# Kernel tuning notes

Measured on AMD Instinct MI355X. Metric: run time of the kernel, lower is better.

Reference implementation:

```python
import jax, jax.numpy as jnp
import numpy as np

N = 8192
F_IN = 512
F_OUT = 512
DENSITY = 0.01


def setup_inputs() -> dict:
    key = jax.random.key(0)
    k_x, k_adj, k_w, k_b = jax.random.split(key, 4)
    input_features = jax.random.normal(k_x, (N, F_IN), dtype=jnp.float32)
    adj = (jax.random.uniform(k_adj, (N, N)) < DENSITY).astype(jnp.float32)
    idx = jnp.arange(N)
    adj = adj.at[idx, idx].set(1.0)
    # nn.Linear(in, out) params; W stored as [in, out] so hidden = x @ W + b
    W = jax.random.normal(k_w, (F_IN, F_OUT), dtype=jnp.float32) / np.sqrt(F_IN)
    b = jax.random.normal(k_b, (F_OUT,), dtype=jnp.float32) * 0.01
    return {"input_features": input_features, "adj": adj, "W": W, "b": b}


def reference(input_features, adj, W, b):
    # adj.to_dense().bool().float(): binarize any nonzero entry
    A = (adj != 0).astype(input_features.dtype)  # [N, N]
    hidden = input_features @ W + b              # [N, F_out]
    deg = jnp.sum(A, axis=0)                     # column sums, [N]
    return (A @ hidden) / deg[:, None]           # [N, F_out]
```

## Files before the change

### kernel.cpp

```cpp
#include <hip/hip_runtime.h>
#include <stdint.h>

#define N_NODES 8192
#define FEAT 512
#define RCAP 192

__device__ __forceinline__ unsigned short f2bf(float f) {
  unsigned int u = __float_as_uint(f);
  u += 0x7fffu + ((u >> 16) & 1u);
  return (unsigned short)(u >> 16);
}
__device__ __forceinline__ float bflo(unsigned int u) { return __uint_as_float(u << 16); }
__device__ __forceinline__ float bfhi(unsigned int u) { return __uint_as_float(u & 0xffff0000u); }

typedef __attribute__((ext_vector_type(8))) short short8;
typedef __attribute__((ext_vector_type(4))) float floatx4;

__global__ __launch_bounds__(256) void prep_kernel(const float* __restrict__ W,
                                                   unsigned short* __restrict__ Wt,
                                                   unsigned int* __restrict__ deg) {
  int gid = blockIdx.x * 256 + threadIdx.x;
  int k = gid >> 9, n = gid & 511;
  Wt[n * 512 + k] = f2bf(W[gid]);
  if (gid < N_NODES) deg[gid] = 0u;
}

__global__ __launch_bounds__(512) void gemm_kernel(const float* __restrict__ x,
                                                   const unsigned short* __restrict__ Wt,
                                                   const float* __restrict__ bias,
                                                   unsigned short* __restrict__ hidden) {
  __shared__ __align__(16) unsigned short Ab[64][40];
  __shared__ __align__(16) unsigned short Bb[256][40];
  int t = threadIdx.x;
  int m0 = blockIdx.x * 64;
  int n0 = blockIdx.y * 256;
  int lane = t & 63, wave = t >> 6;
  int quad = lane >> 4, l15 = lane & 15;
  int wm = wave & 1, wn = wave >> 1;

  floatx4 acc[2][4];
#pragma unroll
  for (int i = 0; i < 2; ++i)
#pragma unroll
    for (int j = 0; j < 4; ++j) acc[i][j] = (floatx4)0.0f;

  int arow = t >> 3, ac = (t & 7) * 4;
  int brow = t >> 1, bc = (t & 1) * 16;
  const float* xa = x + (size_t)(m0 + arow) * 512 + ac;
  const unsigned short* wb = Wt + (size_t)(n0 + brow) * 512 + bc;

  for (int kt = 0; kt < 16; ++kt) {
    int k0 = kt * 32;
    __syncthreads();
    float4 av = *(const float4*)(xa + k0);
    uint2 aw;
    aw.x = (unsigned int)f2bf(av.x) | ((unsigned int)f2bf(av.y) << 16);
    aw.y = (unsigned int)f2bf(av.z) | ((unsigned int)f2bf(av.w) << 16);
    *(uint2*)&Ab[arow][ac] = aw;
    uint4 bv0 = *(const uint4*)(wb + k0);
    uint4 bv1 = *(const uint4*)(wb + k0 + 8);
    *(uint4*)&Bb[brow][bc] = bv0;
    *(uint4*)&Bb[brow][bc + 8] = bv1;
    __syncthreads();

    short8 af[2];
    short8 bfr[4];
#pragma unroll
    for (int im = 0; im < 2; ++im)
      af[im] = *(const short8*)&Ab[wm * 32 + im * 16 + l15][quad * 8];
#pragma unroll
    for (int jn = 0; jn < 4; ++jn)
      bfr[jn] = *(const short8*)&Bb[wn * 64 + jn * 16 + l15][quad * 8];
#pragma unroll
    for (int im = 0; im < 2; ++im)
#pragma unroll
      for (int jn = 0; jn < 4; ++jn)
        acc[im][jn] = __builtin_amdgcn_mfma_f32_16x16x32_bf16(af[im], bfr[jn], acc[im][jn], 0, 0, 0);
  }

#pragma unroll
  for (int jn = 0; jn < 4; ++jn) {
    int col = n0 + wn * 64 + jn * 16 + l15;
    float bb = bias[col];
#pragma unroll
    for (int im = 0; im < 2; ++im) {
#pragma unroll
      for (int rg = 0; rg < 4; ++rg) {
        int row = m0 + wm * 32 + im * 16 + quad * 4 + rg;
        hidden[(size_t)row * 512 + col] = f2bf(acc[im][jn][rg] + bb);
      }
    }
  }
}

#define SCAN4(cv, CH)                                                         \
  {                                                                           \
    int cbase = (CH) * 256 + 4 * lane;                                        \
    _Pragma("unroll")                                                         \
    for (int e = 0; e < 4; ++e) {                                             \
      float val = (e == 0) ? cv.x : (e == 1) ? cv.y : (e == 2) ? cv.z : cv.w; \
      bool nz = (val != 0.0f);                                                \
      unsigned long long m = __ballot(nz);                                    \
      if (nz) {                                                               \
        atomicAdd(&deg[cbase + e], 1u);                                       \
        int p = qcnt + __popcll(m & lanemask);                                \
        if (p < RCAP) row_idx[p] = (unsigned short)(cbase + e);               \
      }                                                                       \
      qcnt += __popcll(m);                                                    \
    }                                                                         \
  }

__global__ __launch_bounds__(256) void scan_kernel(const float* __restrict__ adj,
                                                   unsigned short* __restrict__ idx,
                                                   int* __restrict__ cnt,
                                                   unsigned int* __restrict__ deg) {
  int tid = threadIdx.x;
  int lane = tid & 63, wave = tid >> 6;
  unsigned long long lanemask = (1ull << lane) - 1ull;
  int r = blockIdx.x * 4 + wave;

  const float4* __restrict__ arow = (const float4*)(adj + ((size_t)r << 13));
  unsigned short* row_idx = idx + (size_t)r * RCAP;
  int qcnt = 0;

  float4 b0 = arow[0 * 64 + lane];
  float4 b1 = arow[1 * 64 + lane];
  float4 b2 = arow[2 * 64 + lane];
  float4 b3 = arow[3 * 64 + lane];
  for (int base = 0; base < 32; base += 4) {
    float4 c0 = b0, c1 = b1, c2 = b2, c3 = b3;
    if (base + 4 < 32) {
      b0 = arow[(base + 4) * 64 + lane];
      b1 = arow[(base + 5) * 64 + lane];
      b2 = arow[(base + 6) * 64 + lane];
      b3 = arow[(base + 7) * 64 + lane];
    }
    SCAN4(c0, base + 0)
    SCAN4(c1, base + 1)
    SCAN4(c2, base + 2)
    SCAN4(c3, base + 3)
  }
  if (lane == 0) cnt[r] = (qcnt < RCAP) ? qcnt : RCAP;
}

__global__ __launch_bounds__(256) void gather_kernel(const unsigned short* __restrict__ idx,
                                                     const int* __restrict__ cnt,
                                                     const unsigned int* __restrict__ deg,
                                                     const unsigned short* __restrict__ hidden,
                                                     float* __restrict__ out) {
  int tid = threadIdx.x;
  int lane = tid & 63, wave = tid >> 6;
  int r = blockIdx.x * 4 + wave;

  const unsigned short* ri = idx + (size_t)r * RCAP;
  int n = cnt[r];
  float acc[8] = {0.f, 0.f, 0.f, 0.f, 0.f, 0.f, 0.f, 0.f};

  uint4 iq = *(const uint4*)ri;
  int i = 0;
  for (; i + 8 <= n; i += 8) {
    uint4 iqn;
    if (i + 16 <= n) iqn = *(const uint4*)(ri + i + 8);
    int j[8];
    j[0] = iq.x & 0xffff; j[1] = iq.x >> 16;
    j[2] = iq.y & 0xffff; j[3] = iq.y >> 16;
    j[4] = iq.z & 0xffff; j[5] = iq.z >> 16;
    j[6] = iq.w & 0xffff; j[7] = iq.w >> 16;
    uint4 h[8];
#pragma unroll
    for (int d = 0; d < 8; ++d)
      h[d] = ((const uint4*)(hidden + ((size_t)j[d] << 9)))[lane];
#pragma unroll
    for (int d = 0; d < 8; ++d) {
      acc[0] += bflo(h[d].x); acc[1] += bfhi(h[d].x);
      acc[2] += bflo(h[d].y); acc[3] += bfhi(h[d].y);
      acc[4] += bflo(h[d].z); acc[5] += bfhi(h[d].z);
      acc[6] += bflo(h[d].w); acc[7] += bfhi(h[d].w);
    }
    iq = iqn;
  }
  for (; i < n; ++i) {
    int j = ri[i];
    uint4 h = ((const uint4*)(hidden + ((size_t)j << 9)))[lane];
    acc[0] += bflo(h.x); acc[1] += bfhi(h.x);
    acc[2] += bflo(h.y); acc[3] += bfhi(h.y);
    acc[4] += bflo(h.z); acc[5] += bfhi(h.z);
    acc[6] += bflo(h.w); acc[7] += bfhi(h.w);
  }

  float inv = 1.0f / (float)deg[r];
  float* orow = out + ((size_t)r << 9) + 8 * lane;
  *(float4*)orow       = make_float4(acc[0] * inv, acc[1] * inv, acc[2] * inv, acc[3] * inv);
  *(float4*)(orow + 4) = make_float4(acc[4] * inv, acc[5] * inv, acc[6] * inv, acc[7] * inv);
}

extern "C" void kernel_launch(void* const* d_in, const int* in_sizes, int n_in,
                              void* d_out, int out_size, void* d_ws, size_t ws_size,
                              hipStream_t stream) {
  const float* x   = (const float*)d_in[0];
  const float* adj = (const float*)d_in[1];
  const float* W   = (const float*)d_in[2];
  const float* b   = (const float*)d_in[3];
  float* out = (float*)d_out;

  char* ws = (char*)d_ws;
  unsigned short* hidden = (unsigned short*)ws;
  char* p = ws + (size_t)N_NODES * FEAT * 2;
  unsigned short* Wt = (unsigned short*)p;  p += (size_t)FEAT * FEAT * 2;
  unsigned int*   deg = (unsigned int*)p;   p += (size_t)N_NODES * 4;
  int*            cnt = (int*)p;            p += (size_t)N_NODES * 4;
  unsigned short* idx = (unsigned short*)p;

  prep_kernel<<<1024, 256, 0, stream>>>(W, Wt, deg);
  gemm_kernel<<<dim3(128, 2), 512, 0, stream>>>(x, Wt, b, hidden);
  scan_kernel<<<2048, 256, 0, stream>>>(adj, idx, cnt, deg);
  gather_kernel<<<2048, 256, 0, stream>>>(idx, cnt, deg, hidden, out);
}
```

Before: 448.2 us.

## Merge GEMM and adjacency scan into one launch, split gather by feature half

```diff
diff --git a/kernel.cpp b/kernel.cpp
--- a/kernel.cpp
+++ b/kernel.cpp
@@ -15,6 +15,9 @@
 
 typedef __attribute__((ext_vector_type(8))) short short8;
 typedef __attribute__((ext_vector_type(4))) float floatx4;
+typedef __attribute__((ext_vector_type(4))) float fvec4;
+typedef __attribute__((ext_vector_type(4))) unsigned int uvec4;
+typedef __attribute__((ext_vector_type(2))) unsigned int uvec2;
 
 __global__ __launch_bounds__(256) void prep_kernel(const float* __restrict__ W,
                                                    unsigned short* __restrict__ Wt,
@@ -25,16 +28,70 @@
   if (gid < N_NODES) deg[gid] = 0u;
 }
 
-__global__ __launch_bounds__(512) void gemm_kernel(const float* __restrict__ x,
-                                                   const unsigned short* __restrict__ Wt,
-                                                   const float* __restrict__ bias,
-                                                   unsigned short* __restrict__ hidden) {
+#define SCAN4(cv, CH)                                                         \
+  {                                                                           \
+    int cbase = (CH) * 256 + 4 * lane;                                        \
+    _Pragma("unroll")                                                         \
+    for (int e = 0; e < 4; ++e) {                                             \
+      float val = cv[e];                                                      \
+      bool nz = (val != 0.0f);                                                \
+      unsigned long long m = __ballot(nz);                                    \
+      if (nz) {                                                               \
+        atomicAdd(&deg[cbase + e], 1u);                                       \
+        int p = qcnt + __popcll(m & lanemask);                                \
+        if (p < RCAP)                                                         \
+          __builtin_nontemporal_store((unsigned short)(cbase + e),            \
+                                      row_idx + p);                           \
+      }                                                                       \
+      qcnt += __popcll(m);                                                    \
+    }                                                                         \
+  }
+
+__global__ __launch_bounds__(512, 4) void mega_kernel(const float* __restrict__ x,
+                                                      const unsigned short* __restrict__ Wt,
+                                                      const float* __restrict__ bias,
+                                                      unsigned short* __restrict__ hidden,
+                                                      const float* __restrict__ adj,
+                                                      unsigned short* __restrict__ idx,
+                                                      int* __restrict__ cnt,
+                                                      unsigned int* __restrict__ deg) {
   __shared__ __align__(16) unsigned short Ab[64][40];
   __shared__ __align__(16) unsigned short Bb[256][40];
+  int bid = blockIdx.x;
   int t = threadIdx.x;
-  int m0 = blockIdx.x * 64;
-  int n0 = blockIdx.y * 256;
   int lane = t & 63, wave = t >> 6;
+
+  if (bid < 1024) {
+    unsigned long long lanemask = (1ull << lane) - 1ull;
+    int r = bid * 8 + wave;
+    const fvec4* __restrict__ arow = (const fvec4*)(adj + ((size_t)r << 13));
+    unsigned short* row_idx = idx + (size_t)r * RCAP;
+    int qcnt = 0;
+
+    fvec4 b0 = __builtin_nontemporal_load(arow + 0 * 64 + lane);
+    fvec4 b1 = __builtin_nontemporal_load(arow + 1 * 64 + lane);
+    fvec4 b2 = __builtin_nontemporal_load(arow + 2 * 64 + lane);
+    fvec4 b3 = __builtin_nontemporal_load(arow + 3 * 64 + lane);
+    for (int base = 0; base < 32; base += 4) {
+      fvec4 c0 = b0, c1 = b1, c2 = b2, c3 = b3;
+      if (base + 4 < 32) {
+        b0 = __builtin_nontemporal_load(arow + (base + 4) * 64 + lane);
+        b1 = __builtin_nontemporal_load(arow + (base + 5) * 64 + lane);
+        b2 = __builtin_nontemporal_load(arow + (base + 6) * 64 + lane);
+        b3 = __builtin_nontemporal_load(arow + (base + 7) * 64 + lane);
+      }
+      SCAN4(c0, base + 0)
+      SCAN4(c1, base + 1)
+      SCAN4(c2, base + 2)
+      SCAN4(c3, base + 3)
+    }
+    if (lane == 0) cnt[r] = (qcnt < RCAP) ? qcnt : RCAP;
+    return;
+  }
+
+  int gb = bid - 1024;
+  int m0 = (gb >> 1) * 64;
+  int n0 = (gb & 1) * 256;
   int quad = lane >> 4, l15 = lane & 15;
   int wm = wave & 1, wn = wave >> 1;
 
@@ -44,10 +101,10 @@
 #pragma unroll
     for (int j = 0; j < 4; ++j) acc[i][j] = (floatx4)0.0f;
 
-  int arow = t >> 3, ac = (t & 7) * 4;
-  int brow = t >> 1, bc = (t & 1) * 16;
-  const float* xa = x + (size_t)(m0 + arow) * 512 + ac;
-  const unsigned short* wb = Wt + (size_t)(n0 + brow) * 512 + bc;
+  int arow_s = t >> 3, ac = (t & 7) * 4;
+  int brow_s = t >> 1, bc = (t & 1) * 16;
+  const float* xa = x + (size_t)(m0 + arow_s) * 512 + ac;
+  const unsigned short* wb = Wt + (size_t)(n0 + brow_s) * 512 + bc;
 
   for (int kt = 0; kt < 16; ++kt) {
     int k0 = kt * 32;
@@ -56,11 +113,11 @@
     uint2 aw;
     aw.x = (unsigned int)f2bf(av.x) | ((unsigned int)f2bf(av.y) << 16);
     aw.y = (unsigned int)f2bf(av.z) | ((unsigned int)f2bf(av.w) << 16);
-    *(uint2*)&Ab[arow][ac] = aw;
+    *(uint2*)&Ab[arow_s][ac] = aw;
     uint4 bv0 = *(const uint4*)(wb + k0);
     uint4 bv1 = *(const uint4*)(wb + k0 + 8);
-    *(uint4*)&Bb[brow][bc] = bv0;
-    *(uint4*)&Bb[brow][bc + 8] = bv1;
+    *(uint4*)&Bb[brow_s][bc] = bv0;
+    *(uint4*)&Bb[brow_s][bc + 8] = bv1;
     __syncthreads();
 
     short8 af[2];
@@ -93,105 +150,52 @@
   }
 }
 
-#define SCAN4(cv, CH)                                                         \
-  {                                                                           \
-    int cbase = (CH) * 256 + 4 * lane;                                        \
-    _Pragma("unroll")                                                         \
-    for (int e = 0; e < 4; ++e) {                                             \
-      float val = (e == 0) ? cv.x : (e == 1) ? cv.y : (e == 2) ? cv.z : cv.w; \
-      bool nz = (val != 0.0f);                                                \
-      unsigned long long m = __ballot(nz);                                    \
-      if (nz) {                                                               \
-        atomicAdd(&deg[cbase + e], 1u);                                       \
-        int p = qcnt + __popcll(m & lanemask);                                \
-        if (p < RCAP) row_idx[p] = (unsigned short)(cbase + e);               \
-      }                                                                       \
-      qcnt += __popcll(m);                                                    \
-    }                                                                         \
-  }
-
-__global__ __launch_bounds__(256) void scan_kernel(const float* __restrict__ adj,
-                                                   unsigned short* __restrict__ idx,
-                                                   int* __restrict__ cnt,
-                                                   unsigned int* __restrict__ deg) {
-  int tid = threadIdx.x;
-  int lane = tid & 63, wave = tid >> 6;
-  unsigned long long lanemask = (1ull << lane) - 1ull;
-  int r = blockIdx.x * 4 + wave;
-
-  const float4* __restrict__ arow = (const float4*)(adj + ((size_t)r << 13));
-  unsigned short* row_idx = idx + (size_t)r * RCAP;
-  int qcnt = 0;
-
-  float4 b0 = arow[0 * 64 + lane];
-  float4 b1 = arow[1 * 64 + lane];
-  float4 b2 = arow[2 * 64 + lane];
-  float4 b3 = arow[3 * 64 + lane];
-  for (int base = 0; base < 32; base += 4) {
-    float4 c0 = b0, c1 = b1, c2 = b2, c3 = b3;
-    if (base + 4 < 32) {
-      b0 = arow[(base + 4) * 64 + lane];
-      b1 = arow[(base + 5) * 64 + lane];
-      b2 = arow[(base + 6) * 64 + lane];
-      b3 = arow[(base + 7) * 64 + lane];
-    }
-    SCAN4(c0, base + 0)
-    SCAN4(c1, base + 1)
-    SCAN4(c2, base + 2)
-    SCAN4(c3, base + 3)
-  }
-  if (lane == 0) cnt[r] = (qcnt < RCAP) ? qcnt : RCAP;
-}
-
-__global__ __launch_bounds__(256) void gather_kernel(const unsigned short* __restrict__ idx,
-                                                     const int* __restrict__ cnt,
-                                                     const unsigned int* __restrict__ deg,
-                                                     const unsigned short* __restrict__ hidden,
-                                                     float* __restrict__ out) {
+__global__ __launch_bounds__(256, 7) void gather_kernel(const unsigned short* __restrict__ idx,
+                                                        const int* __restrict__ cnt,
+                                                        const unsigned int* __restrict__ deg,
+                                                        const unsigned short* __restrict__ hidden,
+                                                        float* __restrict__ out,
+                                                        int half) {
   int tid = threadIdx.x;
   int lane = tid & 63, wave = tid >> 6;
   int r = blockIdx.x * 4 + wave;
 
   const unsigned short* ri = idx + (size_t)r * RCAP;
   int n = cnt[r];
-  float acc[8] = {0.f, 0.f, 0.f, 0.f, 0.f, 0.f, 0.f, 0.f};
-
-  uint4 iq = *(const uint4*)ri;
+  float a0 = 0.f, a1 = 0.f, a2 = 0.f, a3 = 0.f;
+  const unsigned short* hbase = hidden + (half << 8) + 4 * lane;
+
+  uvec4 iq = __builtin_nontemporal_load((const uvec4*)ri);
   int i = 0;
   for (; i + 8 <= n; i += 8) {
-    uint4 iqn;
-    if (i + 16 <= n) iqn = *(const uint4*)(ri + i + 8);
+    uvec4 iqn = iq;
+    if (i + 16 <= n) iqn = __builtin_nontemporal_load((const uvec4*)(ri + i + 8));
     int j[8];
     j[0] = iq.x & 0xffff; j[1] = iq.x >> 16;
     j[2] = iq.y & 0xffff; j[3] = iq.y >> 16;
     j[4] = iq.z & 0xffff; j[5] = iq.z >> 16;
     j[6] = iq.w & 0xffff; j[7] = iq.w >> 16;
-    uint4 h[8];
+    uvec2 h[8];
 #pragma unroll
     for (int d = 0; d < 8; ++d)
-      h[d] = ((const uint4*)(hidden + ((size_t)j[d] << 9)))[lane];
+      h[d] = *(const uvec2*)(hbase + ((size_t)j[d] << 9));
 #pragma unroll
     for (int d = 0; d < 8; ++d) {
-      acc[0] += bflo(h[d].x); acc[1] += bfhi(h[d].x);
-      acc[2] += bflo(h[d].y); acc[3] += bfhi(h[d].y);
-      acc[4] += bflo(h[d].z); acc[5] += bfhi(h[d].z);
-      acc[6] += bflo(h[d].w); acc[7] += bfhi(h[d].w);
+      a0 += bflo(h[d].x); a1 += bfhi(h[d].x);
+      a2 += bflo(h[d].y); a3 += bfhi(h[d].y);
     }
     iq = iqn;
   }
   for (; i < n; ++i) {
     int j = ri[i];
-    uint4 h = ((const uint4*)(hidden + ((size_t)j << 9)))[lane];
-    acc[0] += bflo(h.x); acc[1] += bfhi(h.x);
-    acc[2] += bflo(h.y); acc[3] += bfhi(h.y);
-    acc[4] += bflo(h.z); acc[5] += bfhi(h.z);
-    acc[6] += bflo(h.w); acc[7] += bfhi(h.w);
+    uvec2 h = *(const uvec2*)(hbase + ((size_t)j << 9));
+    a0 += bflo(h.x); a1 += bfhi(h.x);
+    a2 += bflo(h.y); a3 += bfhi(h.y);
   }
 
   float inv = 1.0f / (float)deg[r];
-  float* orow = out + ((size_t)r << 9) + 8 * lane;
-  *(float4*)orow       = make_float4(acc[0] * inv, acc[1] * inv, acc[2] * inv, acc[3] * inv);
-  *(float4*)(orow + 4) = make_float4(acc[4] * inv, acc[5] * inv, acc[6] * inv, acc[7] * inv);
+  fvec4 o; o.x = a0 * inv; o.y = a1 * inv; o.z = a2 * inv; o.w = a3 * inv;
+  __builtin_nontemporal_store(o, (fvec4*)(out + ((size_t)r << 9) + (half << 8) + 4 * lane));
 }
 
 extern "C" void kernel_launch(void* const* d_in, const int* in_sizes, int n_in,
@@ -212,7 +216,7 @@
   unsigned short* idx = (unsigned short*)p;
 
   prep_kernel<<<1024, 256, 0, stream>>>(W, Wt, deg);
-  gemm_kernel<<<dim3(128, 2), 512, 0, stream>>>(x, Wt, b, hidden);
-  scan_kernel<<<2048, 256, 0, stream>>>(adj, idx, cnt, deg);
-  gather_kernel<<<2048, 256, 0, stream>>>(idx, cnt, deg, hidden, out);
-}
+  mega_kernel<<<1280, 512, 0, stream>>>(x, Wt, b, hidden, adj, idx, cnt, deg);
+  gather_kernel<<<2048, 256, 0, stream>>>(idx, cnt, deg, hidden, out, 0);
+  gather_kernel<<<2048, 256, 0, stream>>>(idx, cnt, deg, hidden, out, 1);
+}
```

After: 448.5 us. No clear change (+0.1%).
